# Kernel tuning notes

Measured on AMD Instinct MI355X. Metric: run time of the kernel, lower is better.

Reference implementation:

```python
import jax, jax.numpy as jnp
import numpy as np

N, E, D_IN, D_OUT = 16384, 4096, 256, 256


def _leaky(v):
    return jnp.where(v > 0, v, 0.1 * v)


def setup_inputs() -> dict:
    key = jax.random.key(0)
    ks = jax.random.split(key, 8)
    x = jax.random.normal(ks[0], (N, D_IN), dtype=jnp.float32)
    # 0/1 incidence mask, float32 (as multiplied in the torch code)
    H_shape = jax.random.randint(ks[1], (N, E), 0, 2).astype(jnp.float32)
    w1 = jax.random.normal(ks[2], (D_IN, D_OUT), dtype=jnp.float32)
    w2 = jax.random.normal(ks[3], (D_OUT, D_OUT), dtype=jnp.float32)
    a1 = jax.random.normal(ks[4], (D_OUT, 1), dtype=jnp.float32)
    a21 = jax.random.normal(ks[5], (D_OUT, 1), dtype=jnp.float32)
    a22 = jax.random.normal(ks[6], (D_OUT, 1), dtype=jnp.float32)
    return {"x": x, "H_shape": H_shape, "w1": w1, "w2": w2,
            "a1": a1, "a21": a21, "a22": a22}


def reference(x, H_shape, w1, w2, a1, a21, a22):
    xw1 = x @ w1                                  # [N, D]
    # node->edge attention (masked softmax-like over nodes, axis -2)
    f = _leaky(xw1) @ a1                          # [N, 1]
    e = jnp.exp(jnp.tanh(f / 8) * 8) * H_shape    # [N, E]
    e = e / jnp.sum(e, axis=-2, keepdims=True)    # normalize over nodes
    # edge features
    f = _leaky(e.T @ xw1)                         # [E, D]
    # edge->node attention (masked normalize over edges, axis -1)
    b = (_leaky(f @ w2) @ a21).T + _leaky(xw1) @ a22  # [1,E] + [N,1] -> [N,E]
    b = jnp.exp(jnp.tanh(b / 8) * 8) * H_shape
    b = b / jnp.sum(b, axis=-1, keepdims=True)
    return _leaky(b @ f @ w2)                     # [N, D]
```

## Files before the change

kernel.cpp:

```cpp
#include <hip/hip_runtime.h>


typedef __attribute__((ext_vector_type(8))) short short8;
typedef __attribute__((ext_vector_type(4))) float f32x4;
typedef __attribute__((ext_vector_type(4))) int int4v;
typedef __attribute__((ext_vector_type(4))) unsigned int uint4v;

__device__ __forceinline__ float leakyf(float v) { return v > 0.f ? v : 0.1f * v; }
__device__ __forceinline__ float fastrcp(float x) { return __builtin_amdgcn_rcpf(x); }

__device__ __forceinline__ float satexpf(float t) {
    float u = fminf(fmaxf(t * 0.25f, -30.f), 30.f);
    float p = __expf(u);
    float th = (p - 1.f) * fastrcp(p + 1.f);
    return __expf(8.f * th);
}

__device__ __forceinline__ short f2b(float v) {
    unsigned int x = __float_as_uint(v);
    x += 0x7fffu + ((x >> 16) & 1u);
    return (short)(x >> 16);
}
__device__ __forceinline__ float b2f(short s) {
    return __uint_as_float(((unsigned int)(unsigned short)s) << 16);
}
__device__ __forceinline__ unsigned int bits4_to_bytes(unsigned int s) {
    return ((s & 0xFu) * 0x00204081u) & 0x01010101u;
}

__global__ __launch_bounds__(256) void transpose_split2(
        const float* __restrict__ s0, short* __restrict__ dh0, short* __restrict__ dl0,
        const float* __restrict__ s1, short* __restrict__ dh1, short* __restrict__ dl1) {
    const float* src = blockIdx.z ? s1 : s0;
    short* dh = blockIdx.z ? dh1 : dh0;
    short* dl = blockIdx.z ? dl1 : dl0;
    __shared__ float Ts[64][65];
    const int t = threadIdx.x;
    const long r0 = (long)blockIdx.x * 64;
    const long c0 = (long)blockIdx.y * 64;
    {
        const int row = t >> 2, cc = (t & 3) * 16;
        const float* p = src + (r0 + row) * 256 + c0 + cc;
#pragma unroll
        for (int i = 0; i < 4; ++i) {
            f32x4 v = *reinterpret_cast<const f32x4*>(p + i * 4);
#pragma unroll
            for (int k = 0; k < 4; ++k) Ts[row][cc + i * 4 + k] = v[k];
        }
    }
    __syncthreads();
    {
        const int cl = t >> 2, ch = (t & 3) * 16;
        short8 h0, h1, l0, l1;
#pragma unroll
        for (int i = 0; i < 8; ++i) {
            float v = Ts[ch + i][cl];
            short h = f2b(v);
            h0[i] = h; l0[i] = f2b(v - b2f(h));
        }
#pragma unroll
        for (int i = 0; i < 8; ++i) {
            float v = Ts[ch + 8 + i][cl];
            short h = f2b(v);
            h1[i] = h; l1[i] = f2b(v - b2f(h));
        }
        short* qh = dh + (c0 + cl) * 256 + r0 + ch;
        short* ql = dl + (c0 + cl) * 256 + r0 + ch;
        *reinterpret_cast<short8*>(qh) = h0;
        *reinterpret_cast<short8*>(qh + 8) = h1;
        *reinterpret_cast<short8*>(ql) = l0;
        *reinterpret_cast<short8*>(ql + 8) = l1;
    }
}

__global__ __launch_bounds__(256) void transposeH_pack(
        const float* __restrict__ H, unsigned int* __restrict__ Hbits,
        unsigned int* __restrict__ HbitsT) {
    __shared__ float Ts[64][65];
    const int t = threadIdx.x;
    const long r0 = (long)blockIdx.x * 64;
    const long c0 = (long)blockIdx.y * 64;
    {
        const int row = t >> 2, cc = (t & 3) * 16;
        const float* p = H + (r0 + row) * 4096L + c0 + cc;
#pragma unroll
        for (int i = 0; i < 4; ++i) {
            f32x4 v = *reinterpret_cast<const f32x4*>(p + i * 4);
#pragma unroll
            for (int k = 0; k < 4; ++k) Ts[row][cc + i * 4 + k] = v[k];
        }
    }
    __syncthreads();
    if (t < 128) {
        const int nl = t >> 1, w = t & 1;
        unsigned int u = 0;
#pragma unroll
        for (int b = 0; b < 32; ++b)
            u |= (Ts[nl][w * 32 + b] != 0.f ? 1u : 0u) << b;
        Hbits[(r0 + nl) * 128 + (c0 >> 5) + w] = u;
    } else {
        const int t2 = t - 128;
        const int jl = t2 >> 1, w = t2 & 1;
        unsigned int u = 0;
#pragma unroll
        for (int b = 0; b < 32; ++b)
            u |= (Ts[w * 32 + b][jl] != 0.f ? 1u : 0u) << b;
        HbitsT[(c0 + jl) * 512 + (r0 >> 5) + w] = u;
    }
}

__global__ __launch_bounds__(256) void gemm_xw1(
        const float* __restrict__ A, const short* __restrict__ Bh,
        const short* __restrict__ Bl, float* __restrict__ C) {
    __shared__ short Ash[128][72];
    __shared__ short Asl[128][72];
    __shared__ short Bsh[64][72];
    __shared__ short Bsl[64][72];
    const int t = threadIdx.x;
    const int wid = t >> 6, lane = t & 63;
    const int wm = wid & 1, wn = wid >> 1;
    const int quad = lane >> 4, l15 = lane & 15;
    const long m0 = (long)blockIdx.x * 128;
    const long n0 = (long)blockIdx.y * 64;
    f32x4 acc[4][2];
#pragma unroll
    for (int i = 0; i < 4; ++i)
#pragma unroll
        for (int j = 0; j < 2; ++j)
#pragma unroll
            for (int r = 0; r < 4; ++r) acc[i][j][r] = 0.f;

    for (int kb = 0; kb < 256; kb += 64) {
#pragma unroll
        for (int it = 0; it < 4; ++it) {
            const int cid = t + it * 256;
            const int row = cid >> 3, c8 = (cid & 7) * 8;
            const float* ap = A + (m0 + row) * 256 + kb + c8;
            f32x4 v0 = *reinterpret_cast<const f32x4*>(ap);
            f32x4 v1 = *reinterpret_cast<const f32x4*>(ap + 4);
            short8 hi, lo;
#pragma unroll
            for (int k = 0; k < 4; ++k) {
                short h0 = f2b(v0[k]); hi[k] = h0; lo[k] = f2b(v0[k] - b2f(h0));
                short h1 = f2b(v1[k]); hi[4 + k] = h1; lo[4 + k] = f2b(v1[k] - b2f(h1));
            }
            *reinterpret_cast<short8*>(&Ash[row][c8]) = hi;
            *reinterpret_cast<short8*>(&Asl[row][c8]) = lo;
        }
#pragma unroll
        for (int it = 0; it < 2; ++it) {
            const int cid = t + it * 256;
            const int row = cid >> 3, c8 = (cid & 7) * 8;
            *reinterpret_cast<short8*>(&Bsh[row][c8]) =
                *reinterpret_cast<const short8*>(Bh + (n0 + row) * 256 + kb + c8);
            *reinterpret_cast<short8*>(&Bsl[row][c8]) =
                *reinterpret_cast<const short8*>(Bl + (n0 + row) * 256 + kb + c8);
        }
        __syncthreads();
#pragma unroll
        for (int ks = 0; ks < 2; ++ks) {
            short8 ah[4], al[4], bh[2], bl[2];
#pragma unroll
            for (int i = 0; i < 4; ++i) {
                ah[i] = *reinterpret_cast<const short8*>(&Ash[wm * 64 + i * 16 + l15][ks * 32 + quad * 8]);
                al[i] = *reinterpret_cast<const short8*>(&Asl[wm * 64 + i * 16 + l15][ks * 32 + quad * 8]);
            }
#pragma unroll
            for (int j = 0; j < 2; ++j) {
                bh[j] = *reinterpret_cast<const short8*>(&Bsh[wn * 32 + j * 16 + l15][ks * 32 + quad * 8]);
                bl[j] = *reinterpret_cast<const short8*>(&Bsl[wn * 32 + j * 16 + l15][ks * 32 + quad * 8]);
            }
#pragma unroll
            for (int i = 0; i < 4; ++i)
#pragma unroll
                for (int j = 0; j < 2; ++j) {
                    acc[i][j] = __builtin_amdgcn_mfma_f32_16x16x32_bf16(ah[i], bh[j], acc[i][j], 0, 0, 0);
                    acc[i][j] = __builtin_amdgcn_mfma_f32_16x16x32_bf16(ah[i], bl[j], acc[i][j], 0, 0, 0);
                    acc[i][j] = __builtin_amdgcn_mfma_f32_16x16x32_bf16(al[i], bh[j], acc[i][j], 0, 0, 0);
                }
        }
        __syncthreads();
    }
#pragma unroll
    for (int i = 0; i < 4; ++i) {
        const long grow = m0 + wm * 64 + i * 16 + quad * 4;
#pragma unroll
        for (int j = 0; j < 2; ++j) {
            const long gcol = n0 + wn * 32 + j * 16 + l15;
#pragma unroll
            for (int r = 0; r < 4; ++r)
                C[(grow + r) * 256 + gcol] = acc[i][j][r];
        }
    }
}

__global__ __launch_bounds__(256) void node_stats1(
        const float* __restrict__ xw1, const float* __restrict__ a1,
        const float* __restrict__ a22, float* __restrict__ g_out,
        float* __restrict__ dn, unsigned int* __restrict__ ddmax) {
    __shared__ float Mx[4][260];
    const int t = threadIdx.x;
    const int n0 = blockIdx.x * 64;
    const int r = t >> 2, q = t & 3;
    const long n = n0 + r;
    const float* xp = xw1 + n * 256 + q * 64;
    float vals[64];
    float facc = 0.f, dacc = 0.f;
#pragma unroll
    for (int i = 0; i < 16; ++i) {
        f32x4 v  = *reinterpret_cast<const f32x4*>(xp + i * 4);
        f32x4 b1 = *reinterpret_cast<const f32x4*>(a1 + q * 64 + i * 4);
        f32x4 b2 = *reinterpret_cast<const f32x4*>(a22 + q * 64 + i * 4);
#pragma unroll
        for (int k = 0; k < 4; ++k) {
            float lv = leakyf(v[k]);
            facc += lv * b1[k];
            dacc += lv * b2[k];
            vals[i * 4 + k] = v[k];
        }
    }
    facc += __shfl_xor(facc, 1); facc += __shfl_xor(facc, 2);
    dacc += __shfl_xor(dacc, 1); dacc += __shfl_xor(dacc, 2);
    const float g = satexpf(facc);
    if (q == 0) { dn[n] = dacc; g_out[n] = g; }
    float lm[64];
#pragma unroll
    for (int i = 0; i < 64; ++i) lm[i] = fabsf(vals[i] * g);
#pragma unroll
    for (int m = 4; m < 64; m <<= 1)
#pragma unroll
        for (int i = 0; i < 64; ++i) lm[i] = fmaxf(lm[i], __shfl_xor(lm[i], m));
    float gm = g;
#pragma unroll
    for (int m = 1; m < 64; m <<= 1) gm = fmaxf(gm, __shfl_xor(gm, m));
    const int wv = t >> 6, lane = t & 63;
    if (lane < 4) {
#pragma unroll
        for (int i = 0; i < 64; ++i) Mx[wv][lane * 64 + i] = lm[i];
    }
    if (lane == 0) Mx[wv][256] = gm;
    __syncthreads();
    if (t < 256) {
        float m = fmaxf(fmaxf(Mx[0][t], Mx[1][t]), fmaxf(Mx[2][t], Mx[3][t]));
        atomicMax(&ddmax[t], __float_as_uint(m));
    }
    if (t == 0) {
        float m = fmaxf(fmaxf(Mx[0][256], Mx[1][256]), fmaxf(Mx[2][256], Mx[3][256]));
        atomicMax(&ddmax[256], __float_as_uint(m));
    }
}

__global__ __launch_bounds__(256) void quantize_y(
        const float* __restrict__ xw1, const float* __restrict__ g_in,
        const unsigned int* __restrict__ ddmax, char* __restrict__ yQ) {
    __shared__ unsigned int Qh[257][16];
    __shared__ unsigned int Ql[257][16];
    const int t = threadIdx.x;
    const int n0 = blockIdx.x * 64;
    const int dd0 = (t >> 4) * 16;
    const int w = t & 15;
    const int r4 = w * 4;
    float s[16];
#pragma unroll
    for (int i = 0; i < 16; ++i)
        s[i] = 32512.f / __uint_as_float(ddmax[dd0 + i]);
    const float sg = 32512.f / __uint_as_float(ddmax[256]);
    unsigned int bh[16], bl[16];
#pragma unroll
    for (int i = 0; i < 16; ++i) { bh[i] = 0u; bl[i] = 0u; }
    unsigned int gh = 0u, gl = 0u;
#pragma unroll
    for (int rr = 0; rr < 4; ++rr) {
        const long n = n0 + r4 + rr;
        const float gg = g_in[n];
        const float* xp = xw1 + n * 256 + dd0;
#pragma unroll
        for (int c = 0; c < 4; ++c) {
            f32x4 v = *reinterpret_cast<const f32x4*>(xp + c * 4);
#pragma unroll
            for (int k = 0; k < 4; ++k) {
                const int i = c * 4 + k;
                int qv = __float2int_rn(v[k] * gg * s[i]);
                qv = max(-32639, min(32639, qv));
                const int qh = (qv + 128) >> 8;
                const int ql = qv - (qh << 8);
                bh[i] |= ((unsigned int)(qh & 255)) << (8 * rr);
                bl[i] |= ((unsigned int)(ql & 255)) << (8 * rr);
            }
        }
        if (t < 16) {
            int qv = __float2int_rn(gg * sg);
            qv = max(-32639, min(32639, qv));
            const int qh = (qv + 128) >> 8;
            const int ql = qv - (qh << 8);
            gh |= ((unsigned int)(qh & 255)) << (8 * rr);
            gl |= ((unsigned int)(ql & 255)) << (8 * rr);
        }
    }
#pragma unroll
    for (int i = 0; i < 16; ++i) { Qh[dd0 + i][w] = bh[i]; Ql[dd0 + i][w] = bl[i]; }
    if (t < 16) { Qh[256][t] = gh; Ql[256][t] = gl; }
    __syncthreads();
#pragma unroll
    for (int it = 0; it < 2; ++it) {
        const int dd = it * 256 + t;
        if (dd < 288) {
#pragma unroll
            for (int s2 = 0; s2 < 4; ++s2) {
                uint4v vh, vl;
                if (dd < 257) {
                    vh = *reinterpret_cast<const uint4v*>(&Qh[dd][s2 * 4]);
                    vl = *reinterpret_cast<const uint4v*>(&Ql[dd][s2 * 4]);
                } else {
#pragma unroll
                    for (int k = 0; k < 4; ++k) { vh[k] = 0u; vl[k] = 0u; }
                }
                *reinterpret_cast<uint4v*>(yQ + (long)dd * 16384 + n0 + s2 * 16) = vh;
                *reinterpret_cast<uint4v*>(yQ + (long)(288 + dd) * 16384 + n0 + s2 * 16) = vl;
            }
        }
    }
}

__global__ __launch_bounds__(256) void gemm_c1_bits(
        const unsigned int* __restrict__ HbitsT, const char* __restrict__ Bb,
        float* __restrict__ Cp) {
    __shared__ char As[256][144];
    __shared__ char Bsh[48][144];
    __shared__ char Bsl[48][144];
    const int t = threadIdx.x;
    const int wid = t >> 6, lane = t & 63;
    const int quad = lane >> 4, l15 = lane & 15;
    const long m0 = (long)blockIdx.x * 256;
    const long n0 = (long)blockIdx.y * 48;
    const long k0 = (long)blockIdx.z * 4096;
    float* Cz = Cp + (long)blockIdx.z * (4096L * 288);
    int4v acch[4][3], accl[4][3];
#pragma unroll
    for (int i = 0; i < 4; ++i)
#pragma unroll
        for (int j = 0; j < 3; ++j)
#pragma unroll
            for (int r = 0; r < 4; ++r) { acch[i][j][r] = 0; accl[i][j][r] = 0; }

    for (int kb = 0; kb < 4096; kb += 128) {
        {
            uint4v bv = *reinterpret_cast<const uint4v*>(
                    HbitsT + (m0 + t) * 512 + ((k0 + kb) >> 5));
#pragma unroll
            for (int w4 = 0; w4 < 4; ++w4) {
                const unsigned int u = bv[w4];
                uint4v e0, e1;
#pragma unroll
                for (int k = 0; k < 4; ++k) e0[k] = bits4_to_bytes(u >> (4 * k));
#pragma unroll
                for (int k = 0; k < 4; ++k) e1[k] = bits4_to_bytes(u >> (16 + 4 * k));
                *reinterpret_cast<uint4v*>(&As[t][w4 * 32]) = e0;
                *reinterpret_cast<uint4v*>(&As[t][w4 * 32 + 16]) = e1;
            }
        }
#pragma unroll
        for (int it = 0; it < 3; ++it) {
            const int cid = t + it * 256;
            const int idx = (cid < 384) ? cid : cid - 384;
            const int row = idx >> 3, seg = (idx & 7) * 16;
            char* dst = (cid >= 384) ? &Bsl[row][seg] : &Bsh[row][seg];
            const long srow = (cid >= 384) ? (288 + n0 + row) : (n0 + row);
            *reinterpret_cast<uint4v*>(dst) =
                *reinterpret_cast<const uint4v*>(Bb + srow * 16384 + k0 + kb + seg);
        }
        __syncthreads();
#pragma unroll
        for (int ks = 0; ks < 2; ++ks) {
            int4v af[4], bh[3], bl[3];
#pragma unroll
            for (int i = 0; i < 4; ++i)
                af[i] = *reinterpret_cast<const int4v*>(
                        &As[wid * 64 + i * 16 + l15][ks * 64 + quad * 16]);
#pragma unroll
            for (int j = 0; j < 3; ++j) {
                bh[j] = *reinterpret_cast<const int4v*>(&Bsh[j * 16 + l15][ks * 64 + quad * 16]);
                bl[j] = *reinterpret_cast<const int4v*>(&Bsl[j * 16 + l15][ks * 64 + quad * 16]);
            }
#pragma unroll
            for (int i = 0; i < 4; ++i)
#pragma unroll
                for (int j = 0; j < 3; ++j) {
                    acch[i][j] = __builtin_amdgcn_mfma_i32_16x16x64_i8(af[i], bh[j], acch[i][j], 0, 0, 0);
                    accl[i][j] = __builtin_amdgcn_mfma_i32_16x16x64_i8(af[i], bl[j], accl[i][j], 0, 0, 0);
                }
        }
        __syncthreads();
    }
#pragma unroll
    for (int i = 0; i < 4; ++i) {
        const long grow = m0 + wid * 64 + i * 16 + quad * 4;
#pragma unroll
        for (int j = 0; j < 3; ++j) {
            const long gcol = n0 + j * 16 + l15;
#pragma unroll
            for (int r = 0; r < 4; ++r)
                Cz[(grow + r) * 288 + gcol] =
                    256.f * (float)acch[i][j][r] + (float)accl[i][j][r];
        }
    }
}

__global__ __launch_bounds__(256) void reduce_C1(
        const float* __restrict__ C1p, const unsigned int* __restrict__ ddmax,
        float* __restrict__ C1) {
    const int i = blockIdx.x * 256 + threadIdx.x;
    const int dd = i % 288;
    float s = 0.f;
#pragma unroll
    for (int z = 0; z < 4; ++z) s += C1p[(long)z * 4096 * 288 + i];
    C1[i] = s * (__uint_as_float(ddmax[dd]) * (1.f / 32512.f));
}

__global__ __launch_bounds__(256) void gemm_G(
        const float* __restrict__ C1, const short* __restrict__ w2Th,
        const short* __restrict__ w2Tl, const float* __restrict__ a21,
        short* __restrict__ GT, float* __restrict__ cat) {
    __shared__ short Ash[64][72];
    __shared__ short Asl[64][72];
    __shared__ short Bsh[64][72];
    __shared__ short Bsl[64][72];
    __shared__ float Gs[64][65];
    const int t = threadIdx.x;
    const int wid = t >> 6, lane = t & 63;
    const int wm = wid & 1, wn = wid >> 1;
    const int quad = lane >> 4, l15 = lane & 15;
    const long j0 = (long)blockIdx.x * 64;
    const long d0 = (long)blockIdx.y * 64;
    f32x4 acc[2][2];
#pragma unroll
    for (int i = 0; i < 2; ++i)
#pragma unroll
        for (int j = 0; j < 2; ++j)
#pragma unroll
            for (int r = 0; r < 4; ++r) acc[i][j][r] = 0.f;

    for (int kb = 0; kb < 256; kb += 64) {
#pragma unroll
        for (int it = 0; it < 2; ++it) {
            const int cid = t + it * 256;
            const int row = cid >> 3, c8 = (cid & 7) * 8;
            const float rd = fastrcp(C1[(j0 + row) * 288 + 256]);
            const float* ap = C1 + (j0 + row) * 288 + kb + c8;
            f32x4 v0 = *reinterpret_cast<const f32x4*>(ap);
            f32x4 v1 = *reinterpret_cast<const f32x4*>(ap + 4);
            short8 hi, lo;
#pragma unroll
            for (int k = 0; k < 4; ++k) {
                float f0 = leakyf(v0[k] * rd);
                float f1 = leakyf(v1[k] * rd);
                short h0 = f2b(f0); hi[k] = h0; lo[k] = f2b(f0 - b2f(h0));
                short h1 = f2b(f1); hi[4 + k] = h1; lo[4 + k] = f2b(f1 - b2f(h1));
            }
            *reinterpret_cast<short8*>(&Ash[row][c8]) = hi;
            *reinterpret_cast<short8*>(&Asl[row][c8]) = lo;
            *reinterpret_cast<short8*>(&Bsh[row][c8]) =
                *reinterpret_cast<const short8*>(w2Th + (d0 + row) * 256 + kb + c8);
            *reinterpret_cast<short8*>(&Bsl[row][c8]) =
                *reinterpret_cast<const short8*>(w2Tl + (d0 + row) * 256 + kb + c8);
        }
        __syncthreads();
#pragma unroll
        for (int ks = 0; ks < 2; ++ks) {
            short8 ah[2], al[2], bh[2], bl[2];
#pragma unroll
            for (int i = 0; i < 2; ++i) {
                ah[i] = *reinterpret_cast<const short8*>(&Ash[wm * 32 + i * 16 + l15][ks * 32 + quad * 8]);
                al[i] = *reinterpret_cast<const short8*>(&Asl[wm * 32 + i * 16 + l15][ks * 32 + quad * 8]);
            }
#pragma unroll
            for (int j = 0; j < 2; ++j) {
                bh[j] = *reinterpret_cast<const short8*>(&Bsh[wn * 32 + j * 16 + l15][ks * 32 + quad * 8]);
                bl[j] = *reinterpret_cast<const short8*>(&Bsl[wn * 32 + j * 16 + l15][ks * 32 + quad * 8]);
            }
#pragma unroll
            for (int i = 0; i < 2; ++i)
#pragma unroll
                for (int j = 0; j < 2; ++j) {
                    acc[i][j] = __builtin_amdgcn_mfma_f32_16x16x32_bf16(ah[i], bh[j], acc[i][j], 0, 0, 0);
                    acc[i][j] = __builtin_amdgcn_mfma_f32_16x16x32_bf16(ah[i], bl[j], acc[i][j], 0, 0, 0);
                    acc[i][j] = __builtin_amdgcn_mfma_f32_16x16x32_bf16(al[i], bh[j], acc[i][j], 0, 0, 0);
                }
        }
        __syncthreads();
    }
#pragma unroll
    for (int i = 0; i < 2; ++i)
#pragma unroll
        for (int j = 0; j < 2; ++j)
#pragma unroll
            for (int r = 0; r < 4; ++r)
                Gs[wm * 32 + i * 16 + quad * 4 + r][wn * 32 + j * 16 + l15] = acc[i][j][r];
    __syncthreads();
    {
        const int jl = t >> 2, q = t & 3;
        float cp = 0.f;
#pragma unroll
        for (int i = 0; i < 16; ++i) {
            const int d = q * 16 + i;
            cp += leakyf(Gs[jl][d]) * a21[d0 + d];
        }
        cp += __shfl_xor(cp, 1); cp += __shfl_xor(cp, 2);
        if (q == 0) atomicAdd(&cat[j0 + jl], cp);
    }
    {
        const int dl = t >> 2, q = t & 3;
        short8 pk0, pk1;
#pragma unroll
        for (int i = 0; i < 8; ++i) pk0[i] = f2b(Gs[q * 16 + i][dl]);
#pragma unroll
        for (int i = 0; i < 8; ++i) pk1[i] = f2b(Gs[q * 16 + 8 + i][dl]);
        short* gp = GT + (d0 + dl) * 4096 + j0 + q * 16;
        *reinterpret_cast<short8*>(gp) = pk0;
        *reinterpret_cast<short8*>(gp + 8) = pk1;
    }
}

__global__ __launch_bounds__(512) void fused_out(
        const unsigned int* __restrict__ Hbits, const float* __restrict__ cat,
        const float* __restrict__ dn, const short* __restrict__ GT,
        float* __restrict__ out) {
    __shared__ short As[64][72];
    __shared__ short Bs[256][72];
    __shared__ float rsS[64][8];
    __shared__ float rinvS[64];
    const int t = threadIdx.x;
    const int wid = t >> 6, lane = t & 63;
    const int wm = wid >> 2, wn = wid & 3;
    const int quad = lane >> 4, l15 = lane & 15;
    const long m0 = (long)blockIdx.x * 64;
    const int r = lane, jc8 = wid;
    const float drow = dn[m0 + r];
    const int bc = jc8 >> 2;
    const int bo = (jc8 & 3) * 8;

    f32x4 acc[2][4];
#pragma unroll
    for (int i = 0; i < 2; ++i)
#pragma unroll
        for (int j = 0; j < 4; ++j)
#pragma unroll
            for (int x = 0; x < 4; ++x) acc[i][j][x] = 0.f;
    float racc = 0.f;

    for (int kb2 = 0; kb2 < 4096; kb2 += 128) {
        const uint4v bw = *reinterpret_cast<const uint4v*>(
                Hbits + (m0 + r) * 128 + (kb2 >> 5));
#pragma unroll
        for (int half = 0; half < 2; ++half) {
            const int kb = kb2 + half * 64;
#pragma unroll
            for (int it = 0; it < 4; ++it) {
                const int cid = t + it * 512;
                const int row = cid >> 3, c8 = (cid & 7) * 8;
                *reinterpret_cast<short8*>(&Bs[row][c8]) =
                    *reinterpret_cast<const short8*>(GT + row * 4096 + kb + c8);
            }
            {
                const unsigned int w = bw[half * 2 + bc];
                f32x4 cv0 = *reinterpret_cast<const f32x4*>(cat + kb + jc8 * 8);
                f32x4 cv1 = *reinterpret_cast<const f32x4*>(cat + kb + jc8 * 8 + 4);
                short8 pk;
#pragma unroll
                for (int k = 0; k < 8; ++k) {
                    const float cvk = (k < 4) ? cv0[k & 3] : cv1[k & 3];
                    const float s = ((w >> (bo + k)) & 1u) ? satexpf(cvk + drow) : 0.f;
                    const short sb = f2b(s);
                    pk[k] = sb;
                    racc += b2f(sb);
                }
                *reinterpret_cast<short8*>(&As[r][jc8 * 8]) = pk;
            }
            __syncthreads();
#pragma unroll
            for (int ks = 0; ks < 2; ++ks) {
                short8 af[2], bf[4];
#pragma unroll
                for (int i = 0; i < 2; ++i)
                    af[i] = *reinterpret_cast<const short8*>(
                            &As[wm * 32 + i * 16 + l15][ks * 32 + quad * 8]);
#pragma unroll
                for (int j = 0; j < 4; ++j)
                    bf[j] = *reinterpret_cast<const short8*>(
                            &Bs[wn * 64 + j * 16 + l15][ks * 32 + quad * 8]);
#pragma unroll
                for (int i = 0; i < 2; ++i)
#pragma unroll
                    for (int j = 0; j < 4; ++j)
                        acc[i][j] = __builtin_amdgcn_mfma_f32_16x16x32_bf16(
                                af[i], bf[j], acc[i][j], 0, 0, 0);
            }
            __syncthreads();
        }
    }
    rsS[r][jc8] = racc;
    __syncthreads();
    if (t < 64) {
        float s = 0.f;
#pragma unroll
        for (int i = 0; i < 8; ++i) s += rsS[t][i];
        rinvS[t] = fastrcp(s);
    }
    __syncthreads();
#pragma unroll
    for (int i = 0; i < 2; ++i) {
#pragma unroll
        for (int j = 0; j < 4; ++j) {
            const long gcol = wn * 64 + j * 16 + l15;
#pragma unroll
            for (int x = 0; x < 4; ++x) {
                const int rl = wm * 32 + i * 16 + quad * 4 + x;
                out[(m0 + rl) * 256 + gcol] = leakyf(acc[i][j][x] * rinvS[rl]);
            }
        }
    }
}

extern "C" void kernel_launch(void* const* d_in, const int* in_sizes, int n_in,
                              void* d_out, int out_size, void* d_ws, size_t ws_size,
                              hipStream_t stream) {
    const float* x   = (const float*)d_in[0];
    const float* H   = (const float*)d_in[1];
    const float* w1  = (const float*)d_in[2];
    const float* w2  = (const float*)d_in[3];
    const float* a1  = (const float*)d_in[4];
    const float* a21 = (const float*)d_in[5];
    const float* a22 = (const float*)d_in[6];
    float* out = (float*)d_out;
    char* ws = (char*)d_ws;

    float* xw1   = (float*)(ws + 0);
    float* C1p   = (float*)(ws + 0);
    char*  yQ    = (char*)(ws + 67108864);
    float* dn    = (float*)(ws + 76546048);
    float* g     = (float*)(ws + 76611584);
    unsigned int* ddmax = (unsigned int*)(ws + 76677120);
    short* w1Th  = (short*)(ws + 76681216);
    short* w1Tl  = (short*)(ws + 76812288);
    short* w2Th  = (short*)(ws + 76943360);
    short* w2Tl  = (short*)(ws + 77074432);
    float* C1    = (float*)(ws + 77205504);
    short* GT    = (short*)(ws + 81924096);
    float* cat   = (float*)(ws + 84021248);
    unsigned int* Hbits  = (unsigned int*)(ws + 84037632);
    unsigned int* HbitsT = (unsigned int*)(ws + 92426240);

    hipMemsetAsync(ddmax, 0, 288 * sizeof(unsigned int), stream);
    hipMemsetAsync(cat, 0, 4096 * sizeof(float), stream);

    transpose_split2<<<dim3(4, 4, 2), 256, 0, stream>>>(
            w1, w1Th, w1Tl, w2, w2Th, w2Tl);
    transposeH_pack<<<dim3(256, 64), 256, 0, stream>>>(H, Hbits, HbitsT);

    gemm_xw1<<<dim3(128, 4), 256, 0, stream>>>(x, w1Th, w1Tl, xw1);
    node_stats1<<<dim3(256), 256, 0, stream>>>(xw1, a1, a22, g, dn, ddmax);
    quantize_y<<<dim3(256), 256, 0, stream>>>(xw1, g, ddmax, yQ);

    gemm_c1_bits<<<dim3(16, 6, 4), 256, 0, stream>>>(HbitsT, yQ, C1p);
    reduce_C1<<<dim3(4608), 256, 0, stream>>>(C1p, ddmax, C1);

    gemm_G<<<dim3(64, 4), 256, 0, stream>>>(C1, w2Th, w2Tl, a21, GT, cat);

    fused_out<<<dim3(256), 512, 0, stream>>>(Hbits, cat, dn, GT, out);
}
```

Baseline: 675.6 us.

## Double split-K in bit GEMM and halve row tile in fused output kernel

gemm_c1_bits now splits the K dimension into 8 chunks instead of 4, so 768 blocks launch instead of 384, and reduce_C1 sums 8 partial slices. fused_out now handles 32 rows per block instead of 64, so 512 blocks launch instead of 256, with one MFMA row tile per wave and 4-element packing of the attention weights. The goal is to fill more of the GPU's compute units and hide latency better. The cost is twice the partial-sum traffic and workspace for C1p, and twice the reads of GT, since each smaller block reloads the full GT operand with less reuse per load.

New measurement: 642.7 us. 4.9% less time.

```diff
diff --git a/kernel.cpp b/kernel.cpp
--- a/kernel.cpp
+++ b/kernel.cpp
@@ -2,6 +2,7 @@
 
 
 typedef __attribute__((ext_vector_type(8))) short short8;
+typedef __attribute__((ext_vector_type(4))) short short4v;
 typedef __attribute__((ext_vector_type(4))) float f32x4;
 typedef __attribute__((ext_vector_type(4))) int int4v;
 typedef __attribute__((ext_vector_type(4))) unsigned int uint4v;
@@ -333,7 +334,7 @@
     const int quad = lane >> 4, l15 = lane & 15;
     const long m0 = (long)blockIdx.x * 256;
     const long n0 = (long)blockIdx.y * 48;
-    const long k0 = (long)blockIdx.z * 4096;
+    const long k0 = (long)blockIdx.z * 2048;
     float* Cz = Cp + (long)blockIdx.z * (4096L * 288);
     int4v acch[4][3], accl[4][3];
 #pragma unroll
@@ -343,7 +344,7 @@
 #pragma unroll
             for (int r = 0; r < 4; ++r) { acch[i][j][r] = 0; accl[i][j][r] = 0; }
 
-    for (int kb = 0; kb < 4096; kb += 128) {
+    for (int kb = 0; kb < 2048; kb += 128) {
         {
             uint4v bv = *reinterpret_cast<const uint4v*>(
                     HbitsT + (m0 + t) * 512 + ((k0 + kb) >> 5));
@@ -413,7 +414,7 @@
     const int dd = i % 288;
     float s = 0.f;
 #pragma unroll
-    for (int z = 0; z < 4; ++z) s += C1p[(long)z * 4096 * 288 + i];
+    for (int z = 0; z < 8; ++z) s += C1p[(long)z * 4096 * 288 + i];
     C1[i] = s * (__uint_as_float(ddmax[dd]) * (1.f / 32512.f));
 }
 
@@ -525,98 +526,80 @@
         const unsigned int* __restrict__ Hbits, const float* __restrict__ cat,
         const float* __restrict__ dn, const short* __restrict__ GT,
         float* __restrict__ out) {
-    __shared__ short As[64][72];
+    __shared__ short As[32][72];
     __shared__ short Bs[256][72];
-    __shared__ float rsS[64][8];
-    __shared__ float rinvS[64];
+    __shared__ float rsS[32][16];
+    __shared__ float rinvS[32];
     const int t = threadIdx.x;
     const int wid = t >> 6, lane = t & 63;
     const int wm = wid >> 2, wn = wid & 3;
     const int quad = lane >> 4, l15 = lane & 15;
-    const long m0 = (long)blockIdx.x * 64;
-    const int r = lane, jc8 = wid;
+    const long m0 = (long)blockIdx.x * 32;
+    const int r = t & 31, c4 = t >> 5;
     const float drow = dn[m0 + r];
-    const int bc = jc8 >> 2;
-    const int bo = (jc8 & 3) * 8;
-
-    f32x4 acc[2][4];
-#pragma unroll
-    for (int i = 0; i < 2; ++i)
-#pragma unroll
-        for (int j = 0; j < 4; ++j)
-#pragma unroll
-            for (int x = 0; x < 4; ++x) acc[i][j][x] = 0.f;
+    const int bo = (c4 & 7) * 4;
+
+    f32x4 acc[4];
+#pragma unroll
+    for (int j = 0; j < 4; ++j)
+#pragma unroll
+        for (int x = 0; x < 4; ++x) acc[j][x] = 0.f;
     float racc = 0.f;
 
-    for (int kb2 = 0; kb2 < 4096; kb2 += 128) {
-        const uint4v bw = *reinterpret_cast<const uint4v*>(
-                Hbits + (m0 + r) * 128 + (kb2 >> 5));
-#pragma unroll
-        for (int half = 0; half < 2; ++half) {
-            const int kb = kb2 + half * 64;
-#pragma unroll
-            for (int it = 0; it < 4; ++it) {
-                const int cid = t + it * 512;
-                const int row = cid >> 3, c8 = (cid & 7) * 8;
-                *reinterpret_cast<short8*>(&Bs[row][c8]) =
-                    *reinterpret_cast<const short8*>(GT + row * 4096 + kb + c8);
-            }
-            {
-                const unsigned int w = bw[half * 2 + bc];
-                f32x4 cv0 = *reinterpret_cast<const f32x4*>(cat + kb + jc8 * 8);
-                f32x4 cv1 = *reinterpret_cast<const f32x4*>(cat + kb + jc8 * 8 + 4);
-                short8 pk;
-#pragma unroll
-                for (int k = 0; k < 8; ++k) {
-                    const float cvk = (k < 4) ? cv0[k & 3] : cv1[k & 3];
-                    const float s = ((w >> (bo + k)) & 1u) ? satexpf(cvk + drow) : 0.f;
-                    const short sb = f2b(s);
-                    pk[k] = sb;
-                    racc += b2f(sb);
-                }
-                *reinterpret_cast<short8*>(&As[r][jc8 * 8]) = pk;
-            }
-            __syncthreads();
-#pragma unroll
-            for (int ks = 0; ks < 2; ++ks) {
-                short8 af[2], bf[4];
-#pragma unroll
-                for (int i = 0; i < 2; ++i)
-                    af[i] = *reinterpret_cast<const short8*>(
-                            &As[wm * 32 + i * 16 + l15][ks * 32 + quad * 8]);
-#pragma unroll
-                for (int j = 0; j < 4; ++j)
-                    bf[j] = *reinterpret_cast<const short8*>(
-                            &Bs[wn * 64 + j * 16 + l15][ks * 32 + quad * 8]);
-#pragma unroll
-                for (int i = 0; i < 2; ++i)
-#pragma unroll
-                    for (int j = 0; j < 4; ++j)
-                        acc[i][j] = __builtin_amdgcn_mfma_f32_16x16x32_bf16(
-                                af[i], bf[j], acc[i][j], 0, 0, 0);
-            }
-            __syncthreads();
-        }
-    }
-    rsS[r][jc8] = racc;
+    for (int kb = 0; kb < 4096; kb += 64) {
+#pragma unroll
+        for (int it = 0; it < 4; ++it) {
+            const int cid = t + it * 512;
+            const int row = cid >> 3, c8 = (cid & 7) * 8;
+            *reinterpret_cast<short8*>(&Bs[row][c8]) =
+                *reinterpret_cast<const short8*>(GT + row * 4096 + kb + c8);
+        }
+        {
+            const unsigned int w = Hbits[(m0 + r) * 128 + (kb >> 5) + (c4 >> 3)];
+            f32x4 cv = *reinterpret_cast<const f32x4*>(cat + kb + c4 * 4);
+            short4v pk;
+#pragma unroll
+            for (int k = 0; k < 4; ++k) {
+                const float s = ((w >> (bo + k)) & 1u) ? satexpf(cv[k] + drow) : 0.f;
+                const short sb = f2b(s);
+                pk[k] = sb;
+                racc += b2f(sb);
+            }
+            *reinterpret_cast<short4v*>(&As[r][c4 * 4]) = pk;
+        }
+        __syncthreads();
+#pragma unroll
+        for (int ks = 0; ks < 2; ++ks) {
+            short8 af, bf[4];
+            af = *reinterpret_cast<const short8*>(
+                    &As[wm * 16 + l15][ks * 32 + quad * 8]);
+#pragma unroll
+            for (int j = 0; j < 4; ++j)
+                bf[j] = *reinterpret_cast<const short8*>(
+                        &Bs[wn * 64 + j * 16 + l15][ks * 32 + quad * 8]);
+#pragma unroll
+            for (int j = 0; j < 4; ++j)
+                acc[j] = __builtin_amdgcn_mfma_f32_16x16x32_bf16(
+                        af, bf[j], acc[j], 0, 0, 0);
+        }
+        __syncthreads();
+    }
+    rsS[r][c4] = racc;
     __syncthreads();
-    if (t < 64) {
+    if (t < 32) {
         float s = 0.f;
 #pragma unroll
-        for (int i = 0; i < 8; ++i) s += rsS[t][i];
+        for (int i = 0; i < 16; ++i) s += rsS[t][i];
         rinvS[t] = fastrcp(s);
     }
     __syncthreads();
 #pragma unroll
-    for (int i = 0; i < 2; ++i) {
-#pragma unroll
-        for (int j = 0; j < 4; ++j) {
-            const long gcol = wn * 64 + j * 16 + l15;
-#pragma unroll
-            for (int x = 0; x < 4; ++x) {
-                const int rl = wm * 32 + i * 16 + quad * 4 + x;
-                out[(m0 + rl) * 256 + gcol] = leakyf(acc[i][j][x] * rinvS[rl]);
-            }
+    for (int j = 0; j < 4; ++j) {
+        const long gcol = wn * 64 + j * 16 + l15;
+#pragma unroll
+        for (int x = 0; x < 4; ++x) {
+            const int rl = wm * 16 + quad * 4 + x;
+            out[(m0 + rl) * 256 + gcol] = leakyf(acc[j][x] * rinvS[rl]);
         }
     }
 }
@@ -661,10 +644,10 @@
     node_stats1<<<dim3(256), 256, 0, stream>>>(xw1, a1, a22, g, dn, ddmax);
     quantize_y<<<dim3(256), 256, 0, stream>>>(xw1, g, ddmax, yQ);
 
-    gemm_c1_bits<<<dim3(16, 6, 4), 256, 0, stream>>>(HbitsT, yQ, C1p);
+    gemm_c1_bits<<<dim3(16, 6, 8), 256, 0, stream>>>(HbitsT, yQ, C1p);
     reduce_C1<<<dim3(4608), 256, 0, stream>>>(C1p, ddmax, C1);
 
     gemm_G<<<dim3(64, 4), 256, 0, stream>>>(C1, w2Th, w2Tl, a21, GT, cat);
 
-    fused_out<<<dim3(256), 512, 0, stream>>>(Hbits, cat, dn, GT, out);
-}
+    fused_out<<<dim3(512), 512, 0, stream>>>(Hbits, cat, dn, GT, out);
+}
```

## Split-K the output and C1 GEMMs and fold memsets into the pack kernel

Applied to the files above, without the earlier changes.

The final attention-weighted GEMM is split four ways along the edge dimension. The launch grows from 256 to 1024 blocks of 512 threads. Each split writes partial outputs and row sums, and a new combine_out kernel reduces them, normalizes and applies leaky-ReLU. gemm_c1_bits uses 8 K-splits instead of 4 to raise parallelism, and the two hipMemsetAsync calls are replaced by zeroing inside transposeH_pack. The intent is to fill all CUs in the tail kernels at the cost of roughly 64 MB of extra partial-sum traffic, one extra launch, and a larger workspace footprint.

Result: faster. 616.3 us (-8.8%).

```diff
diff --git a/kernel.cpp b/kernel.cpp
--- a/kernel.cpp
+++ b/kernel.cpp
@@ -2,6 +2,7 @@
 
 
 typedef __attribute__((ext_vector_type(8))) short short8;
+typedef __attribute__((ext_vector_type(4))) short short4v;
 typedef __attribute__((ext_vector_type(4))) float f32x4;
 typedef __attribute__((ext_vector_type(4))) int int4v;
 typedef __attribute__((ext_vector_type(4))) unsigned int uint4v;
@@ -75,11 +76,18 @@
 
 __global__ __launch_bounds__(256) void transposeH_pack(
         const float* __restrict__ H, unsigned int* __restrict__ Hbits,
-        unsigned int* __restrict__ HbitsT) {
+        unsigned int* __restrict__ HbitsT, unsigned int* __restrict__ ddmax,
+        float* __restrict__ cat) {
     __shared__ float Ts[64][65];
     const int t = threadIdx.x;
     const long r0 = (long)blockIdx.x * 64;
     const long c0 = (long)blockIdx.y * 64;
+    if (blockIdx.x == 0 && blockIdx.y == 0) {
+        if (t < 256) ddmax[t] = 0u;
+        if (t < 32) ddmax[256 + t] = 0u;
+#pragma unroll
+        for (int i = 0; i < 16; ++i) cat[t * 16 + i] = 0.f;
+    }
     {
         const int row = t >> 2, cc = (t & 3) * 16;
         const float* p = H + (r0 + row) * 4096L + c0 + cc;
@@ -333,7 +341,7 @@
     const int quad = lane >> 4, l15 = lane & 15;
     const long m0 = (long)blockIdx.x * 256;
     const long n0 = (long)blockIdx.y * 48;
-    const long k0 = (long)blockIdx.z * 4096;
+    const long k0 = (long)blockIdx.z * 2048;
     float* Cz = Cp + (long)blockIdx.z * (4096L * 288);
     int4v acch[4][3], accl[4][3];
 #pragma unroll
@@ -343,7 +351,7 @@
 #pragma unroll
             for (int r = 0; r < 4; ++r) { acch[i][j][r] = 0; accl[i][j][r] = 0; }
 
-    for (int kb = 0; kb < 4096; kb += 128) {
+    for (int kb = 0; kb < 2048; kb += 128) {
         {
             uint4v bv = *reinterpret_cast<const uint4v*>(
                     HbitsT + (m0 + t) * 512 + ((k0 + kb) >> 5));
@@ -413,7 +421,7 @@
     const int dd = i % 288;
     float s = 0.f;
 #pragma unroll
-    for (int z = 0; z < 4; ++z) s += C1p[(long)z * 4096 * 288 + i];
+    for (int z = 0; z < 8; ++z) s += C1p[(long)z * 4096 * 288 + i];
     C1[i] = s * (__uint_as_float(ddmax[dd]) * (1.f / 32512.f));
 }
 
@@ -521,23 +529,23 @@
     }
 }
 
-__global__ __launch_bounds__(512) void fused_out(
+__global__ __launch_bounds__(512, 4) void fused_out_split(
         const unsigned int* __restrict__ Hbits, const float* __restrict__ cat,
         const float* __restrict__ dn, const short* __restrict__ GT,
-        float* __restrict__ out) {
+        float* __restrict__ outP, float* __restrict__ rsP) {
     __shared__ short As[64][72];
     __shared__ short Bs[256][72];
     __shared__ float rsS[64][8];
-    __shared__ float rinvS[64];
     const int t = threadIdx.x;
     const int wid = t >> 6, lane = t & 63;
     const int wm = wid >> 2, wn = wid & 3;
     const int quad = lane >> 4, l15 = lane & 15;
     const long m0 = (long)blockIdx.x * 64;
-    const int r = lane, jc8 = wid;
+    const int z = blockIdx.y;
+    const int kbase = z * 1024;
+    const int r = t & 63, c8 = t >> 6;
     const float drow = dn[m0 + r];
-    const int bc = jc8 >> 2;
-    const int bo = (jc8 & 3) * 8;
+    const int bo = (c8 & 3) * 8;
 
     f32x4 acc[2][4];
 #pragma unroll
@@ -548,65 +556,60 @@
             for (int x = 0; x < 4; ++x) acc[i][j][x] = 0.f;
     float racc = 0.f;
 
-    for (int kb2 = 0; kb2 < 4096; kb2 += 128) {
-        const uint4v bw = *reinterpret_cast<const uint4v*>(
-                Hbits + (m0 + r) * 128 + (kb2 >> 5));
-#pragma unroll
-        for (int half = 0; half < 2; ++half) {
-            const int kb = kb2 + half * 64;
-#pragma unroll
-            for (int it = 0; it < 4; ++it) {
-                const int cid = t + it * 512;
-                const int row = cid >> 3, c8 = (cid & 7) * 8;
-                *reinterpret_cast<short8*>(&Bs[row][c8]) =
-                    *reinterpret_cast<const short8*>(GT + row * 4096 + kb + c8);
-            }
-            {
-                const unsigned int w = bw[half * 2 + bc];
-                f32x4 cv0 = *reinterpret_cast<const f32x4*>(cat + kb + jc8 * 8);
-                f32x4 cv1 = *reinterpret_cast<const f32x4*>(cat + kb + jc8 * 8 + 4);
-                short8 pk;
-#pragma unroll
-                for (int k = 0; k < 8; ++k) {
-                    const float cvk = (k < 4) ? cv0[k & 3] : cv1[k & 3];
-                    const float s = ((w >> (bo + k)) & 1u) ? satexpf(cvk + drow) : 0.f;
-                    const short sb = f2b(s);
-                    pk[k] = sb;
-                    racc += b2f(sb);
-                }
-                *reinterpret_cast<short8*>(&As[r][jc8 * 8]) = pk;
-            }
-            __syncthreads();
-#pragma unroll
-            for (int ks = 0; ks < 2; ++ks) {
-                short8 af[2], bf[4];
-#pragma unroll
-                for (int i = 0; i < 2; ++i)
-                    af[i] = *reinterpret_cast<const short8*>(
-                            &As[wm * 32 + i * 16 + l15][ks * 32 + quad * 8]);
+    for (int kk = 0; kk < 1024; kk += 64) {
+        const int kb = kbase + kk;
+#pragma unroll
+        for (int it = 0; it < 4; ++it) {
+            const int cid = t + it * 512;
+            const int row = cid >> 3, cc = (cid & 7) * 8;
+            *reinterpret_cast<short8*>(&Bs[row][cc]) =
+                *reinterpret_cast<const short8*>(GT + row * 4096 + kb + cc);
+        }
+        {
+            const unsigned int w = Hbits[(m0 + r) * 128 + (kb >> 5) + (c8 >> 2)];
+            f32x4 cv0 = *reinterpret_cast<const f32x4*>(cat + kb + c8 * 8);
+            f32x4 cv1 = *reinterpret_cast<const f32x4*>(cat + kb + c8 * 8 + 4);
+            short8 pk;
+#pragma unroll
+            for (int k = 0; k < 8; ++k) {
+                const float cvk = (k < 4) ? cv0[k & 3] : cv1[k & 3];
+                const float s = ((w >> (bo + k)) & 1u) ? satexpf(cvk + drow) : 0.f;
+                const short sb = f2b(s);
+                pk[k] = sb;
+                racc += b2f(sb);
+            }
+            *reinterpret_cast<short8*>(&As[r][c8 * 8]) = pk;
+        }
+        __syncthreads();
+#pragma unroll
+        for (int ks = 0; ks < 2; ++ks) {
+            short8 af[2], bf[4];
+#pragma unroll
+            for (int i = 0; i < 2; ++i)
+                af[i] = *reinterpret_cast<const short8*>(
+                        &As[wm * 32 + i * 16 + l15][ks * 32 + quad * 8]);
+#pragma unroll
+            for (int j = 0; j < 4; ++j)
+                bf[j] = *reinterpret_cast<const short8*>(
+                        &Bs[wn * 64 + j * 16 + l15][ks * 32 + quad * 8]);
+#pragma unroll
+            for (int i = 0; i < 2; ++i)
 #pragma unroll
                 for (int j = 0; j < 4; ++j)
-                    bf[j] = *reinterpret_cast<const short8*>(
-                            &Bs[wn * 64 + j * 16 + l15][ks * 32 + quad * 8]);
-#pragma unroll
-                for (int i = 0; i < 2; ++i)
-#pragma unroll
-                    for (int j = 0; j < 4; ++j)
-                        acc[i][j] = __builtin_amdgcn_mfma_f32_16x16x32_bf16(
-                                af[i], bf[j], acc[i][j], 0, 0, 0);
-            }
-            __syncthreads();
-        }
-    }
-    rsS[r][jc8] = racc;
+                    acc[i][j] = __builtin_amdgcn_mfma_f32_16x16x32_bf16(
+                            af[i], bf[j], acc[i][j], 0, 0, 0);
+        }
+        __syncthreads();
+    }
+    rsS[r][c8] = racc;
     __syncthreads();
     if (t < 64) {
         float s = 0.f;
 #pragma unroll
         for (int i = 0; i < 8; ++i) s += rsS[t][i];
-        rinvS[t] = fastrcp(s);
-    }
-    __syncthreads();
+        rsP[z * 16384 + m0 + t] = s;
+    }
+    float* op = outP + (long)z * (16384L * 256);
 #pragma unroll
     for (int i = 0; i < 2; ++i) {
 #pragma unroll
@@ -614,11 +617,30 @@
             const long gcol = wn * 64 + j * 16 + l15;
 #pragma unroll
             for (int x = 0; x < 4; ++x) {
-                const int rl = wm * 32 + i * 16 + quad * 4 + x;
-                out[(m0 + rl) * 256 + gcol] = leakyf(acc[i][j][x] * rinvS[rl]);
-            }
-        }
-    }
+                const long grow = m0 + wm * 32 + i * 16 + quad * 4 + x;
+                op[grow * 256 + gcol] = acc[i][j][x];
+            }
+        }
+    }
+}
+
+__global__ __launch_bounds__(256) void combine_out(
+        const float* __restrict__ outP, const float* __restrict__ rsP,
+        float* __restrict__ out) {
+    const long i = ((long)blockIdx.x * 256 + threadIdx.x) * 4;
+    const long n = i >> 8;
+    f32x4 s = *reinterpret_cast<const f32x4*>(outP + i);
+#pragma unroll
+    for (int z = 1; z < 4; ++z) {
+        f32x4 v = *reinterpret_cast<const f32x4*>(outP + (long)z * (16384L * 256) + i);
+#pragma unroll
+        for (int k = 0; k < 4; ++k) s[k] += v[k];
+    }
+    const float rinv = fastrcp(rsP[n] + rsP[16384 + n] + rsP[32768 + n] + rsP[49152 + n]);
+    f32x4 o;
+#pragma unroll
+    for (int k = 0; k < 4; ++k) o[k] = leakyf(s[k] * rinv);
+    *reinterpret_cast<f32x4*>(out + i) = o;
 }
 
 extern "C" void kernel_launch(void* const* d_in, const int* in_sizes, int n_in,
@@ -649,22 +671,22 @@
     float* cat   = (float*)(ws + 84021248);
     unsigned int* Hbits  = (unsigned int*)(ws + 84037632);
     unsigned int* HbitsT = (unsigned int*)(ws + 92426240);
-
-    hipMemsetAsync(ddmax, 0, 288 * sizeof(unsigned int), stream);
-    hipMemsetAsync(cat, 0, 4096 * sizeof(float), stream);
+    float* outP  = (float*)(ws + 134217728);
+    float* rsP   = (float*)(ws + 201326592);
 
     transpose_split2<<<dim3(4, 4, 2), 256, 0, stream>>>(
             w1, w1Th, w1Tl, w2, w2Th, w2Tl);
-    transposeH_pack<<<dim3(256, 64), 256, 0, stream>>>(H, Hbits, HbitsT);
+    transposeH_pack<<<dim3(256, 64), 256, 0, stream>>>(H, Hbits, HbitsT, ddmax, cat);
 
     gemm_xw1<<<dim3(128, 4), 256, 0, stream>>>(x, w1Th, w1Tl, xw1);
     node_stats1<<<dim3(256), 256, 0, stream>>>(xw1, a1, a22, g, dn, ddmax);
     quantize_y<<<dim3(256), 256, 0, stream>>>(xw1, g, ddmax, yQ);
 
-    gemm_c1_bits<<<dim3(16, 6, 4), 256, 0, stream>>>(HbitsT, yQ, C1p);
+    gemm_c1_bits<<<dim3(16, 6, 8), 256, 0, stream>>>(HbitsT, yQ, C1p);
     reduce_C1<<<dim3(4608), 256, 0, stream>>>(C1p, ddmax, C1);
 
     gemm_G<<<dim3(64, 4), 256, 0, stream>>>(C1, w2Th, w2Tl, a21, GT, cat);
 
-    fused_out<<<dim3(256), 512, 0, stream>>>(Hbits, cat, dn, GT, out);
-}
+    fused_out_split<<<dim3(256, 4), 512, 0, stream>>>(Hbits, cat, dn, GT, outP, rsP);
+    combine_out<<<dim3(4096), 256, 0, stream>>>(outP, rsP, out);
+}
```
